# Optimization experiments

Hardware: AMD Instinct MI355X
Metric: run time of the kernel (lower is better)

The kernel has to match this reference:

```python
import jax, jax.numpy as jnp
import numpy as np

L, D, H, HD, FF, V, NH, S = 5, 1024, 8, 128, 4096, 2048, 15, 2
EPS = 1e-6
THETA = 10000.0


def rms_norm(x, w):
    x32 = x.astype(jnp.float32)
    y = x32 * jax.lax.rsqrt(jnp.mean(x32 * x32, axis=-1, keepdims=True) + EPS)
    return (y * w.astype(jnp.float32)).astype(x.dtype)


def rotate_half(x):
    x1, x2 = x[..., : HD // 2], x[..., HD // 2:]
    return jnp.concatenate((-x2, x1), axis=-1)


def setup_inputs() -> dict:
    key = jax.random.key(0)
    ks = jax.random.split(key, 20)
    s = 0.02
    inp = {
        "past_hidden": jax.random.normal(ks[0], (1, 1, D), jnp.float32),
        "cb0_token": jax.random.randint(ks[1], (1, 1), 0, V, jnp.int32),
        "codec_emb": jax.random.normal(ks[2], (V, D), jnp.float32) * s,
        "Wq": jax.random.normal(ks[3], (L, D, H * HD), jnp.float32) * s,
        "Wk": jax.random.normal(ks[4], (L, D, H * HD), jnp.float32) * s,
        "Wv": jax.random.normal(ks[5], (L, D, H * HD), jnp.float32) * s,
        "Wo": jax.random.normal(ks[6], (L, H * HD, D), jnp.float32) * s,
        "q_norm_w": jnp.ones((L, HD), jnp.float32),
        "k_norm_w": jnp.ones((L, HD), jnp.float32),
        "ln1_w": jnp.ones((L, D), jnp.float32),
        "ln2_w": jnp.ones((L, D), jnp.float32),
        "Wgate": jax.random.normal(ks[7], (L, D, FF), jnp.float32) * s,
        "Wup": jax.random.normal(ks[8], (L, D, FF), jnp.float32) * s,
        "Wdown": jax.random.normal(ks[9], (L, FF, D), jnp.float32) * s,
        "final_norm_w": jnp.ones((D,), jnp.float32),
        "lm_heads": jax.random.normal(ks[10], (NH, D, V), jnp.float32) * s,
    }
    return inp


def reference(past_hidden, codec_emb, Wq, Wk, Wv, Wo, q_norm_w, k_norm_w,
              ln1_w, ln2_w, Wgate, Wup, Wdown, final_norm_w, lm_heads,
              cb0_token):
    # Embed CB0 token and build 2-token prefill sequence [1, 2, D].
    cb0_embed = codec_emb[cb0_token]            # [1, 1, D]
    h = jnp.concatenate([past_hidden, cb0_embed], axis=1)

    # Rotary cos/sin for positions [0, 1]: [1, 1, S, HD].
    pos = jnp.arange(S, dtype=jnp.float32)
    inv_freq = 1.0 / (THETA ** (jnp.arange(0, HD, 2, dtype=jnp.float32) / HD))
    freqs = pos[:, None] * inv_freq[None, :]    # [S, HD/2]
    emb = jnp.concatenate([freqs, freqs], axis=-1)
    cos = jnp.cos(emb)[None, None]
    sin = jnp.sin(emb)[None, None]

    causal_mask = jnp.array([[0.0, -1e9], [0.0, 0.0]], jnp.float32)
    scale = 1.0 / np.sqrt(HD)

    def layer_step(h, p):
        wq, wk, wv, wo, qn, kn, l1, l2, wg, wu, wd = p
        res = h
        x = rms_norm(h, l1)                     # [1, S, D]
        q = (x @ wq).reshape(1, S, H, HD)
        k = (x @ wk).reshape(1, S, H, HD)
        v = (x @ wv).reshape(1, S, H, HD)
        q = rms_norm(q, qn)                     # per-head qk-norm
        k = rms_norm(k, kn)
        q = q.transpose(0, 2, 1, 3)             # [1, H, S, HD]
        k = k.transpose(0, 2, 1, 3)
        v = v.transpose(0, 2, 1, 3)
        q = q * cos + rotate_half(q) * sin
        k = k * cos + rotate_half(k) * sin
        attn = jnp.einsum('bhqd,bhkd->bhqk', q, k) * scale + causal_mask
        w = jax.nn.softmax(attn.astype(jnp.float32), axis=-1).astype(q.dtype)
        o = jnp.einsum('bhqk,bhkd->bhqd', w, v)
        o = o.transpose(0, 2, 1, 3).reshape(1, S, H * HD) @ wo
        h = res + o
        res = h
        x = rms_norm(h, l2)
        mlp = (jax.nn.silu(x @ wg) * (x @ wu)) @ wd
        return res + mlp, (k, v)

    h, (ks_, vs_) = jax.lax.scan(
        layer_step, h,
        (Wq, Wk, Wv, Wo, q_norm_w, k_norm_w, ln1_w, ln2_w, Wgate, Wup, Wdown))

    h = rms_norm(h, final_norm_w)
    last = h[:, -1, :]                          # [1, D]
    all_logits = jnp.einsum('bd,ndv->nbv', last, lm_heads)  # [15, 1, V]
    # Interleave keys/values per layer: [2L, 1, H, S, HD].
    kv_cache = jnp.stack([ks_, vs_], axis=1).reshape(2 * L, 1, H, S, HD)
    return all_logits, kv_cache
```

## Files before the change

kernel.cpp:

```cpp
#include <hip/hip_runtime.h>
#include <math.h>

#define EPS 1e-6f
#define FLAGS_OFF 32768


__device__ __forceinline__ float ato(const float* p) {
    return __hip_atomic_load(p, __ATOMIC_RELAXED, __HIP_MEMORY_SCOPE_AGENT);
}

__device__ __forceinline__ float red32(float v) {
#pragma unroll
    for (int m = 16; m >= 1; m >>= 1) v += __shfl_xor(v, m, 64);
    return v;
}

__device__ __forceinline__ void spin_wait(int* flags, int p, int need, int t) {
    if (t < 64) {
        int* base = flags + p * 256;
        while (true) {
            int v = (t < 16) ? __hip_atomic_load(base + t * 16, __ATOMIC_RELAXED,
                                                 __HIP_MEMORY_SCOPE_AGENT) : 0;
#pragma unroll
            for (int m = 8; m >= 1; m >>= 1) v += __shfl_xor(v, m, 64);
            v = __shfl(v, 0, 64);
            if (v >= need) break;
            __builtin_amdgcn_s_sleep(4);
        }
    }
    __syncthreads();
}

__device__ __forceinline__ void task_done(int* flags, int p, int t) {
    asm volatile("s_waitcnt vmcnt(0)" ::: "memory");
    __syncthreads();
    if (t == 0)
        __hip_atomic_fetch_add(flags + p * 256 + (blockIdx.x & 15) * 16, 1,
                               __ATOMIC_RELAXED, __HIP_MEMORY_SCOPE_AGENT);
}

__global__ void init_kernel(const float* __restrict__ past_hidden,
                            const float* __restrict__ codec_emb,
                            const int* __restrict__ tok,
                            float* __restrict__ ws,
                            float* __restrict__ logits)
{
    size_t idx = (size_t)blockIdx.x * blockDim.x + threadIdx.x;
    size_t stride = (size_t)gridDim.x * blockDim.x;
    for (size_t i = idx; i < 30720; i += stride) ws[2048 + i] = 0.f;
    for (size_t i = idx; i < 81920; i += stride) ws[43008 + i] = 0.f;
    for (size_t i = idx; i < 30720; i += stride) logits[i] = 0.f;
    int* flags = (int*)(ws + FLAGS_OFF);
    for (size_t i = idx; i < 20 * 256; i += stride) flags[i] = 0;
    int t = tok[0];
    for (size_t i = idx; i < 1024; i += stride) {
        ws[i]        = past_hidden[i];
        ws[1024 + i] = codec_emb[(size_t)t * 1024 + i];
    }
}

template <int S, int R>
__device__ void phase_gemv(
    float* smem, int t,
    const float* __restrict__ hbuf,
    const float* __restrict__ nw,
    const float* __restrict__ W0, const float* __restrict__ W1,
    const float* __restrict__ W2, size_t w_zstride,
    float* __restrict__ out, int out_sstride, size_t out_zstride, int N,
    int nx, int ny, int nz,
    int* flags, int widx, int wneed, int didx, int start, int nblk)
{
    float* xs = smem;
    float* sstot = smem + S * 1024;
    const int lane = t & 63;
    const int dp = t >> 6;
    const int ntask = nx * ny * nz;
    bool waited = (widx < 0);

    for (int task = (blockIdx.x - start + 2 * nblk) % nblk; task < ntask; task += nblk) {
        const int z = task / (nx * ny);
        const int rem = task - z * (nx * ny);
        const int by = rem / nx;
        const int bx = rem - by * nx;

        const float* W;
        if (W1) W = (z == 0) ? W0 : ((z == 1) ? W1 : W2);
        else    W = W0 + (size_t)z * w_zstride;
        float* outz = out + (size_t)z * out_zstride;

        const int j = bx * 256 + lane * 4;
        const int d0 = by * (4 * R) + dp * R;

        float4 wreg[R];
        const float* Wp = W + (size_t)d0 * N + j;
#pragma unroll
        for (int i = 0; i < R; ++i)
            wreg[i] = *reinterpret_cast<const float4*>(Wp + (size_t)i * N);

        if (!waited) { spin_wait(flags, widx, wneed, t); waited = true; }

        float ss[S];
        {
            float4 nw4 = *reinterpret_cast<const float4*>(nw + t * 4);
#pragma unroll
            for (int s = 0; s < S; ++s) {
                float x0 = ato(hbuf + s * 1024 + t * 4 + 0);
                float x1 = ato(hbuf + s * 1024 + t * 4 + 1);
                float x2 = ato(hbuf + s * 1024 + t * 4 + 2);
                float x3 = ato(hbuf + s * 1024 + t * 4 + 3);
                ss[s] = x0 * x0 + x1 * x1 + x2 * x2 + x3 * x3;
                xs[s * 1024 + t * 4 + 0] = x0 * nw4.x;
                xs[s * 1024 + t * 4 + 1] = x1 * nw4.y;
                xs[s * 1024 + t * 4 + 2] = x2 * nw4.z;
                xs[s * 1024 + t * 4 + 3] = x3 * nw4.w;
            }
        }
        __syncthreads();

        float acc[S][4];
#pragma unroll
        for (int s = 0; s < S; ++s) { acc[s][0] = acc[s][1] = acc[s][2] = acc[s][3] = 0.f; }
#pragma unroll
        for (int i = 0; i < R; ++i) {
            int dd = d0 + i;
#pragma unroll
            for (int s = 0; s < S; ++s) {
                float xv = xs[s * 1024 + dd];
                acc[s][0] += xv * wreg[i].x; acc[s][1] += xv * wreg[i].y;
                acc[s][2] += xv * wreg[i].z; acc[s][3] += xv * wreg[i].w;
            }
        }

#pragma unroll
        for (int s = 0; s < S; ++s) {
            float v = ss[s];
#pragma unroll
            for (int m = 32; m >= 1; m >>= 1) v += __shfl_xor(v, m, 64);
            if (lane == 0) sstot[s * 4 + dp] = v;
        }
        __syncthreads();
        float sc[S];
#pragma unroll
        for (int s = 0; s < S; ++s) {
            float tot = sstot[s * 4 + 0] + sstot[s * 4 + 1] + sstot[s * 4 + 2] + sstot[s * 4 + 3];
            sc[s] = rsqrtf(tot / 1024.f + EPS);
        }

#pragma unroll
        for (int s = 0; s < S; ++s)
#pragma unroll
            for (int c = 0; c < 4; ++c)
                xs[(dp * S + s) * 256 + lane * 4 + c] = acc[s][c] * sc[s];
        __syncthreads();
        for (int o = t; o < S * 256; o += 256) {
            int s = o >> 8;
            int col = o & 255;
            float sum = 0.f;
#pragma unroll
            for (int p = 0; p < 4; ++p) sum += xs[(p * S + s) * 256 + col];
            atomicAdd(outz + (size_t)s * out_sstride + bx * 256 + col, sum);
        }
        if (didx >= 0) task_done(flags, didx, t);
        else __syncthreads();
    }
}

__device__ void phase_attn_o(
    float* smem, int t,
    const float* __restrict__ qkv, const float* __restrict__ qnw,
    const float* __restrict__ knw, const float* __restrict__ W,
    float* __restrict__ out, float* __restrict__ kvc,
    int* flags, int widx, int wneed, int didx, int start, int nblk)
{
    float* xs = smem;
    const int lane = t & 63;
    const int dp = t >> 6;
    bool waited = false;

    for (int task = (blockIdx.x - start + 2 * nblk) % nblk; task < 512; task += nblk) {
        const int bx = task & 3;
        const int by = task >> 2;
        const int j = bx * 256 + lane * 4;
        const int d0 = by * 8 + dp * 2;

        float4 wreg[2];
        const float* Wp = W + (size_t)d0 * 1024 + j;
        wreg[0] = *reinterpret_cast<const float4*>(Wp);
        wreg[1] = *reinterpret_cast<const float4*>(Wp + 1024);

        if (!waited) { spin_wait(flags, widx, wneed, t); waited = true; }

        const int hh = t >> 5;
        const int g = t & 31;
        float q[2][4], k[2][4], v[2][4];
#pragma unroll
        for (int s = 0; s < 2; ++s)
#pragma unroll
            for (int c = 0; c < 4; ++c) {
                int d = g + c * 32;
                q[s][c] = ato(qkv + s * 3072 +        hh * 128 + d);
                k[s][c] = ato(qkv + s * 3072 + 1024 + hh * 128 + d);
                v[s][c] = ato(qkv + s * 3072 + 2048 + hh * 128 + d);
            }
#pragma unroll
        for (int s = 0; s < 2; ++s) {
            float sq = q[s][0]*q[s][0] + q[s][1]*q[s][1] + q[s][2]*q[s][2] + q[s][3]*q[s][3];
            float sk = k[s][0]*k[s][0] + k[s][1]*k[s][1] + k[s][2]*k[s][2] + k[s][3]*k[s][3];
            sq = red32(sq); sk = red32(sk);
            float qsc = rsqrtf(sq / 128.f + EPS);
            float ksc = rsqrtf(sk / 128.f + EPS);
#pragma unroll
            for (int c = 0; c < 4; ++c) {
                q[s][c] *= qsc * qnw[g + c * 32];
                k[s][c] *= ksc * knw[g + c * 32];
            }
        }
        float inv0 = powf(10000.f, -(float)g / 64.f);
        float inv1 = powf(10000.f, -(float)(g + 32) / 64.f);
        float cA = cosf(inv0), sA = sinf(inv0);
        float cB = cosf(inv1), sB = sinf(inv1);
        float q1[4] = { q[1][0]*cA - q[1][2]*sA, q[1][1]*cB - q[1][3]*sB,
                        q[1][2]*cA + q[1][0]*sA, q[1][3]*cB + q[1][1]*sB };
        float k1[4] = { k[1][0]*cA - k[1][2]*sA, k[1][1]*cB - k[1][3]*sB,
                        k[1][2]*cA + k[1][0]*sA, k[1][3]*cB + k[1][1]*sB };

        if (task == 0) {
#pragma unroll
            for (int c = 0; c < 4; ++c) {
                int d = g + c * 32;
                kvc[hh * 256 +       d] = k[0][c];
                kvc[hh * 256 + 128 + d] = k1[c];
                kvc[2048 + hh * 256 +       d] = v[0][c];
                kvc[2048 + hh * 256 + 128 + d] = v[1][c];
            }
        }

        float p00 = red32(q[0][0]*k[0][0] + q[0][1]*k[0][1] + q[0][2]*k[0][2] + q[0][3]*k[0][3]);
        float p01 = red32(q[0][0]*k1[0]   + q[0][1]*k1[1]   + q[0][2]*k1[2]   + q[0][3]*k1[3]);
        float p10 = red32(q1[0]*k[0][0]   + q1[1]*k[0][1]   + q1[2]*k[0][2]   + q1[3]*k[0][3]);
        float p11 = red32(q1[0]*k1[0]     + q1[1]*k1[1]     + q1[2]*k1[2]     + q1[3]*k1[3]);

        const float scale = 0.08838834764831845f;
        float s00 = p00 * scale, s01 = p01 * scale - 1e9f;
        float m0 = fmaxf(s00, s01);
        float e0 = expf(s00 - m0), e1 = expf(s01 - m0);
        float in0 = 1.f / (e0 + e1);
        float w00 = e0 * in0, w01 = e1 * in0;
        float s10 = p10 * scale, s11 = p11 * scale;
        float m1 = fmaxf(s10, s11);
        float f0 = expf(s10 - m1), f1 = expf(s11 - m1);
        float in1 = 1.f / (f0 + f1);
        float w10 = f0 * in1, w11 = f1 * in1;

#pragma unroll
        for (int c = 0; c < 4; ++c) {
            int d = g + c * 32;
            xs[       hh * 128 + d] = w00 * v[0][c] + w01 * v[1][c];
            xs[1024 + hh * 128 + d] = w10 * v[0][c] + w11 * v[1][c];
        }
        __syncthreads();

        float acc[2][4] = {{0.f,0.f,0.f,0.f},{0.f,0.f,0.f,0.f}};
#pragma unroll
        for (int i = 0; i < 2; ++i) {
            int dd = d0 + i;
#pragma unroll
            for (int s = 0; s < 2; ++s) {
                float xv = xs[s * 1024 + dd];
                acc[s][0] += xv * wreg[i].x; acc[s][1] += xv * wreg[i].y;
                acc[s][2] += xv * wreg[i].z; acc[s][3] += xv * wreg[i].w;
            }
        }
        __syncthreads();
#pragma unroll
        for (int s = 0; s < 2; ++s)
#pragma unroll
            for (int c = 0; c < 4; ++c)
                xs[(dp * 2 + s) * 256 + lane * 4 + c] = acc[s][c];
        __syncthreads();
        for (int o = t; o < 512; o += 256) {
            int s = o >> 8, col = o & 255;
            float sum = 0.f;
#pragma unroll
            for (int p = 0; p < 4; ++p) sum += xs[(p * 2 + s) * 256 + col];
            atomicAdd(out + (size_t)s * 1024 + bx * 256 + col, sum);
        }
        task_done(flags, didx, t);
    }
}

__device__ void phase_down(
    float* smem, int t,
    const float* __restrict__ gu, const float* __restrict__ W,
    float* __restrict__ out,
    int* flags, int widx, int wneed, int didx, int start, int nblk)
{
    float* red = smem;
    float* a   = smem + 2048;
    const int lane = t & 63;
    const int dp = t >> 6;
    bool waited = false;

    for (int task = (blockIdx.x - start + 2 * nblk) % nblk; task < 512; task += nblk) {
        const int bx = task & 3;
        const int by = task >> 2;
        const int j = bx * 256 + lane * 4;
        const int f0 = by * 32 + dp * 8;

        float4 wreg[8];
        const float* Wp = W + (size_t)f0 * 1024 + j;
#pragma unroll
        for (int i = 0; i < 8; ++i)
            wreg[i] = *reinterpret_cast<const float4*>(Wp + (size_t)i * 1024);

        if (!waited) { spin_wait(flags, widx, wneed, t); waited = true; }

        if (t < 64) {
            int s = t >> 5, x = t & 31;
            int f = by * 32 + x;
            float g = ato(gu + s * 8192 + f);
            float u = ato(gu + s * 8192 + 4096 + f);
            a[s * 32 + x] = g / (1.f + expf(-g)) * u;
        }
        __syncthreads();

        float acc[2][4] = {{0.f,0.f,0.f,0.f},{0.f,0.f,0.f,0.f}};
#pragma unroll
        for (int i = 0; i < 8; ++i) {
            int dl = dp * 8 + i;
#pragma unroll
            for (int s = 0; s < 2; ++s) {
                float xv = a[s * 32 + dl];
                acc[s][0] += xv * wreg[i].x; acc[s][1] += xv * wreg[i].y;
                acc[s][2] += xv * wreg[i].z; acc[s][3] += xv * wreg[i].w;
            }
        }
        __syncthreads();
#pragma unroll
        for (int s = 0; s < 2; ++s)
#pragma unroll
            for (int c = 0; c < 4; ++c)
                red[(dp * 2 + s) * 256 + lane * 4 + c] = acc[s][c];
        __syncthreads();
        for (int o = t; o < 512; o += 256) {
            int s = o >> 8, col = o & 255;
            float sum = 0.f;
#pragma unroll
            for (int p = 0; p < 4; ++p) sum += red[(p * 2 + s) * 256 + col];
            atomicAdd(out + (size_t)s * 1024 + bx * 256 + col, sum);
        }
        task_done(flags, didx, t);
    }
}

__global__ __launch_bounds__(256, 4) void net_kernel(
    const float* __restrict__ Wq, const float* __restrict__ Wk,
    const float* __restrict__ Wv, const float* __restrict__ Wo,
    const float* __restrict__ qnw, const float* __restrict__ knw,
    const float* __restrict__ ln1, const float* __restrict__ ln2,
    const float* __restrict__ Wg, const float* __restrict__ Wu,
    const float* __restrict__ Wd, const float* __restrict__ fnw,
    const float* __restrict__ lmh,
    float* __restrict__ ws, float* __restrict__ logits, float* __restrict__ kvc)
{
    __shared__ float smem[2112];
    const int t = threadIdx.x;
    const int nblk = gridDim.x;
    float* h    = ws;
    float* qkvb = ws + 2048;
    float* gub  = ws + 43008;
    int* flags  = (int*)(ws + FLAGS_OFF);
    int off = 0;

    for (int l = 0; l < 5; ++l) {
        const float* wq = Wq + (size_t)l * 1024 * 1024;
        const float* wk = Wk + (size_t)l * 1024 * 1024;
        const float* wv = Wv + (size_t)l * 1024 * 1024;
        const float* wo = Wo + (size_t)l * 1024 * 1024;
        const float* wg = Wg + (size_t)l * 1024 * 4096;
        const float* wu = Wu + (size_t)l * 1024 * 4096;
        const float* wd = Wd + (size_t)l * 4096 * 1024;
        float* qkv = qkvb + l * 6144;
        float* gu  = gub  + l * 16384;
        int st;

        st = off % nblk; off += 384;
        phase_gemv<2, 8>(smem, t, h, ln1 + l * 1024, wq, wk, wv, 0,
                         qkv, 3072, 1024, 1024, 4, 32, 3,
                         flags, l ? 4 * (l - 1) + 3 : -1, 512, 4 * l, st, nblk);
        st = off % nblk; off += 512;
        phase_attn_o(smem, t, qkv, qnw + l * 128, knw + l * 128, wo, h,
                     kvc + (size_t)(2 * l) * 2048,
                     flags, 4 * l, 384, 4 * l + 1, st, nblk);
        st = off % nblk; off += 512;
        phase_gemv<2, 16>(smem, t, h, ln2 + l * 1024, wg, wu, wu, 0,
                          gu, 8192, 4096, 4096, 16, 16, 2,
                          flags, 4 * l + 1, 512, 4 * l + 2, st, nblk);
        st = off % nblk; off += 512;
        phase_down(smem, t, gu, wd, h, flags, 4 * l + 2, 512, 4 * l + 3, st, nblk);
    }

    int st = off % nblk;
    phase_gemv<1, 16>(smem, t, h + 1024, fnw, lmh, nullptr, nullptr,
                      (size_t)1024 * 2048, logits, 2048, 2048, 2048,
                      8, 16, 15, flags, 19, 512, -1, st, nblk);
}

extern "C" void kernel_launch(void* const* d_in, const int* in_sizes, int n_in,
                              void* d_out, int out_size, void* d_ws, size_t ws_size,
                              hipStream_t stream)
{
    const float* past_hidden = (const float*)d_in[0];
    const int*   cb0         = (const int*)d_in[1];
    const float* codec_emb   = (const float*)d_in[2];
    const float* Wq  = (const float*)d_in[3];
    const float* Wk  = (const float*)d_in[4];
    const float* Wv  = (const float*)d_in[5];
    const float* Wo  = (const float*)d_in[6];
    const float* qnw = (const float*)d_in[7];
    const float* knw = (const float*)d_in[8];
    const float* ln1 = (const float*)d_in[9];
    const float* ln2 = (const float*)d_in[10];
    const float* Wg  = (const float*)d_in[11];
    const float* Wu  = (const float*)d_in[12];
    const float* Wd  = (const float*)d_in[13];
    const float* fnw = (const float*)d_in[14];
    const float* lmh = (const float*)d_in[15];

    float* ws     = (float*)d_ws;
    float* logits = (float*)d_out;
    float* kvc    = (float*)d_out + 30720;

    init_kernel<<<128, 256, 0, stream>>>(past_hidden, codec_emb, cb0, ws, logits);

    static int nblk = 0;
    if (nblk == 0) {
        int perCU = 0;
        if (hipOccupancyMaxActiveBlocksPerMultiprocessor(&perCU, net_kernel, 256, 0) != hipSuccess
            || perCU < 1) perCU = 1;
        nblk = perCU * 256;
        if (nblk > 1024) nblk = 1024;
        if (nblk < 256) nblk = 256;
    }

    void* args[] = {
        (void*)&Wq, (void*)&Wk, (void*)&Wv, (void*)&Wo,
        (void*)&qnw, (void*)&knw, (void*)&ln1, (void*)&ln2,
        (void*)&Wg, (void*)&Wu, (void*)&Wd, (void*)&fnw, (void*)&lmh,
        (void*)&ws, (void*)&logits, (void*)&kvc
    };
    hipLaunchCooperativeKernel((void*)net_kernel, dim3(nblk), dim3(256),
                               args, 0, stream);
}
```

Before: 566.1 us.

## Switch to dynamic atomic task queues with coarser tiles and split partial residual buffers

Replaces the static round-robin task assignment with per-phase atomic work counters, so blocks claim tasks dynamically. Tiles grow in the QKV, O-projection and down-projection phases, which cuts the number of tasks and flag increments. Residual updates from O and down are split into two partial buffers that later readers sum, spreading atomic contention. The cooperative launch with an occupancy query becomes a plain launch of 1024 blocks and the spin sleep is shortened. This relies on every block in the plain launch being resident to avoid spin-wait deadlock, and the residual bookkeeping through h plus hp needs care to stay correct.

```diff
diff --git a/kernel.cpp b/kernel.cpp
--- a/kernel.cpp
+++ b/kernel.cpp
@@ -2,8 +2,9 @@
 #include <math.h>
 
 #define EPS 1e-6f
-#define FLAGS_OFF 32768
-
+
+#define SYNC_OFF 32768
+#define HP_OFF   38912
 
 __device__ __forceinline__ float ato(const float* p) {
     return __hip_atomic_load(p, __ATOMIC_RELAXED, __HIP_MEMORY_SCOPE_AGENT);
@@ -15,9 +16,9 @@
     return v;
 }
 
-__device__ __forceinline__ void spin_wait(int* flags, int p, int need, int t) {
+__device__ __forceinline__ void spin_wait(int* sync, int widx, int need, int t) {
     if (t < 64) {
-        int* base = flags + p * 256;
+        int* base = sync + 1024 + widx * 256;
         while (true) {
             int v = (t < 16) ? __hip_atomic_load(base + t * 16, __ATOMIC_RELAXED,
                                                  __HIP_MEMORY_SCOPE_AGENT) : 0;
@@ -25,17 +26,17 @@
             for (int m = 8; m >= 1; m >>= 1) v += __shfl_xor(v, m, 64);
             v = __shfl(v, 0, 64);
             if (v >= need) break;
-            __builtin_amdgcn_s_sleep(4);
+            __builtin_amdgcn_s_sleep(1);
         }
     }
     __syncthreads();
 }
 
-__device__ __forceinline__ void task_done(int* flags, int p, int t) {
+__device__ __forceinline__ void task_done(int* sync, int p, int t) {
     asm volatile("s_waitcnt vmcnt(0)" ::: "memory");
     __syncthreads();
     if (t == 0)
-        __hip_atomic_fetch_add(flags + p * 256 + (blockIdx.x & 15) * 16, 1,
+        __hip_atomic_fetch_add(sync + 1024 + p * 256 + (blockIdx.x & 15) * 16, 1,
                                __ATOMIC_RELAXED, __HIP_MEMORY_SCOPE_AGENT);
 }
 
@@ -50,8 +51,9 @@
     for (size_t i = idx; i < 30720; i += stride) ws[2048 + i] = 0.f;
     for (size_t i = idx; i < 81920; i += stride) ws[43008 + i] = 0.f;
     for (size_t i = idx; i < 30720; i += stride) logits[i] = 0.f;
-    int* flags = (int*)(ws + FLAGS_OFF);
-    for (size_t i = idx; i < 20 * 256; i += stride) flags[i] = 0;
+    for (size_t i = idx; i < 4096;  i += stride) ws[HP_OFF + i] = 0.f;
+    int* sync = (int*)(ws + SYNC_OFF);
+    for (size_t i = idx; i < 6144; i += stride) sync[i] = 0;
     int t = tok[0];
     for (size_t i = idx; i < 1024; i += stride) {
         ws[i]        = past_hidden[i];
@@ -62,14 +64,15 @@
 template <int S, int R>
 __device__ void phase_gemv(
     float* smem, int t,
-    const float* __restrict__ hbuf,
+    const float* hbuf, const float* hp,
     const float* __restrict__ nw,
     const float* __restrict__ W0, const float* __restrict__ W1,
     const float* __restrict__ W2, size_t w_zstride,
     float* __restrict__ out, int out_sstride, size_t out_zstride, int N,
     int nx, int ny, int nz,
-    int* flags, int widx, int wneed, int didx, int start, int nblk)
-{
+    int* sync, int phase, int widx, int wneed, int didx)
+{
+    __shared__ int tsk;
     float* xs = smem;
     float* sstot = smem + S * 1024;
     const int lane = t & 63;
@@ -77,7 +80,14 @@
     const int ntask = nx * ny * nz;
     bool waited = (widx < 0);
 
-    for (int task = (blockIdx.x - start + 2 * nblk) % nblk; task < ntask; task += nblk) {
+    while (true) {
+        if (t == 0)
+            tsk = __hip_atomic_fetch_add(sync + phase * 16, 1, __ATOMIC_RELAXED,
+                                         __HIP_MEMORY_SCOPE_AGENT);
+        __syncthreads();
+        const int task = tsk;
+        if (task >= ntask) break;
+
         const int z = task / (nx * ny);
         const int rem = task - z * (nx * ny);
         const int by = rem / nx;
@@ -97,22 +107,29 @@
         for (int i = 0; i < R; ++i)
             wreg[i] = *reinterpret_cast<const float4*>(Wp + (size_t)i * N);
 
-        if (!waited) { spin_wait(flags, widx, wneed, t); waited = true; }
+        if (!waited) { spin_wait(sync, widx, wneed, t); waited = true; }
 
         float ss[S];
         {
             float4 nw4 = *reinterpret_cast<const float4*>(nw + t * 4);
 #pragma unroll
             for (int s = 0; s < S; ++s) {
-                float x0 = ato(hbuf + s * 1024 + t * 4 + 0);
-                float x1 = ato(hbuf + s * 1024 + t * 4 + 1);
-                float x2 = ato(hbuf + s * 1024 + t * 4 + 2);
-                float x3 = ato(hbuf + s * 1024 + t * 4 + 3);
+                int base = s * 1024 + t * 4;
+                float x0 = ato(hbuf + base + 0);
+                float x1 = ato(hbuf + base + 1);
+                float x2 = ato(hbuf + base + 2);
+                float x3 = ato(hbuf + base + 3);
+                if (hp) {
+                    x0 += ato(hp + base + 0) + ato(hp + 2048 + base + 0);
+                    x1 += ato(hp + base + 1) + ato(hp + 2048 + base + 1);
+                    x2 += ato(hp + base + 2) + ato(hp + 2048 + base + 2);
+                    x3 += ato(hp + base + 3) + ato(hp + 2048 + base + 3);
+                }
                 ss[s] = x0 * x0 + x1 * x1 + x2 * x2 + x3 * x3;
-                xs[s * 1024 + t * 4 + 0] = x0 * nw4.x;
-                xs[s * 1024 + t * 4 + 1] = x1 * nw4.y;
-                xs[s * 1024 + t * 4 + 2] = x2 * nw4.z;
-                xs[s * 1024 + t * 4 + 3] = x3 * nw4.w;
+                xs[base + 0] = x0 * nw4.x;
+                xs[base + 1] = x1 * nw4.y;
+                xs[base + 2] = x2 * nw4.z;
+                xs[base + 3] = x3 * nw4.w;
             }
         }
         __syncthreads();
@@ -160,7 +177,7 @@
             for (int p = 0; p < 4; ++p) sum += xs[(p * S + s) * 256 + col];
             atomicAdd(outz + (size_t)s * out_sstride + bx * 256 + col, sum);
         }
-        if (didx >= 0) task_done(flags, didx, t);
+        if (didx >= 0) task_done(sync, didx, t);
         else __syncthreads();
     }
 }
@@ -169,26 +186,37 @@
     float* smem, int t,
     const float* __restrict__ qkv, const float* __restrict__ qnw,
     const float* __restrict__ knw, const float* __restrict__ W,
-    float* __restrict__ out, float* __restrict__ kvc,
-    int* flags, int widx, int wneed, int didx, int start, int nblk)
-{
+    float* __restrict__ hp,
+    float* __restrict__ kvc,
+    int* sync, int phase, int widx, int wneed, int didx)
+{
+    __shared__ int tsk;
     float* xs = smem;
     const int lane = t & 63;
     const int dp = t >> 6;
     bool waited = false;
 
-    for (int task = (blockIdx.x - start + 2 * nblk) % nblk; task < 512; task += nblk) {
+    while (true) {
+        if (t == 0)
+            tsk = __hip_atomic_fetch_add(sync + phase * 16, 1, __ATOMIC_RELAXED,
+                                         __HIP_MEMORY_SCOPE_AGENT);
+        __syncthreads();
+        const int task = tsk;
+        if (task >= 128) break;
+
         const int bx = task & 3;
         const int by = task >> 2;
         const int j = bx * 256 + lane * 4;
-        const int d0 = by * 8 + dp * 2;
-
-        float4 wreg[2];
+        const int d0 = by * 32 + dp * 8;
+        float* out = hp + (by & 1) * 2048;
+
+        float4 wreg[8];
         const float* Wp = W + (size_t)d0 * 1024 + j;
-        wreg[0] = *reinterpret_cast<const float4*>(Wp);
-        wreg[1] = *reinterpret_cast<const float4*>(Wp + 1024);
-
-        if (!waited) { spin_wait(flags, widx, wneed, t); waited = true; }
+#pragma unroll
+        for (int i = 0; i < 8; ++i)
+            wreg[i] = *reinterpret_cast<const float4*>(Wp + (size_t)i * 1024);
+
+        if (!waited) { spin_wait(sync, widx, wneed, t); waited = true; }
 
         const int hh = t >> 5;
         const int g = t & 31;
@@ -262,7 +290,7 @@
 
         float acc[2][4] = {{0.f,0.f,0.f,0.f},{0.f,0.f,0.f,0.f}};
 #pragma unroll
-        for (int i = 0; i < 2; ++i) {
+        for (int i = 0; i < 8; ++i) {
             int dd = d0 + i;
 #pragma unroll
             for (int s = 0; s < 2; ++s) {
@@ -285,52 +313,61 @@
             for (int p = 0; p < 4; ++p) sum += xs[(p * 2 + s) * 256 + col];
             atomicAdd(out + (size_t)s * 1024 + bx * 256 + col, sum);
         }
-        task_done(flags, didx, t);
+        task_done(sync, didx, t);
     }
 }
 
 __device__ void phase_down(
     float* smem, int t,
     const float* __restrict__ gu, const float* __restrict__ W,
-    float* __restrict__ out,
-    int* flags, int widx, int wneed, int didx, int start, int nblk)
-{
+    float* __restrict__ hp,
+    int* sync, int phase, int widx, int wneed, int didx)
+{
+    __shared__ int tsk;
     float* red = smem;
     float* a   = smem + 2048;
     const int lane = t & 63;
     const int dp = t >> 6;
     bool waited = false;
 
-    for (int task = (blockIdx.x - start + 2 * nblk) % nblk; task < 512; task += nblk) {
+    while (true) {
+        if (t == 0)
+            tsk = __hip_atomic_fetch_add(sync + phase * 16, 1, __ATOMIC_RELAXED,
+                                         __HIP_MEMORY_SCOPE_AGENT);
+        __syncthreads();
+        const int task = tsk;
+        if (task >= 256) break;
+
         const int bx = task & 3;
         const int by = task >> 2;
         const int j = bx * 256 + lane * 4;
-        const int f0 = by * 32 + dp * 8;
-
-        float4 wreg[8];
+        const int f0 = by * 64 + dp * 16;
+        float* out = hp + (by & 1) * 2048;
+
+        float4 wreg[16];
         const float* Wp = W + (size_t)f0 * 1024 + j;
 #pragma unroll
-        for (int i = 0; i < 8; ++i)
+        for (int i = 0; i < 16; ++i)
             wreg[i] = *reinterpret_cast<const float4*>(Wp + (size_t)i * 1024);
 
-        if (!waited) { spin_wait(flags, widx, wneed, t); waited = true; }
-
-        if (t < 64) {
-            int s = t >> 5, x = t & 31;
-            int f = by * 32 + x;
+        if (!waited) { spin_wait(sync, widx, wneed, t); waited = true; }
+
+        if (t < 128) {
+            int s = t >> 6, x = t & 63;
+            int f = by * 64 + x;
             float g = ato(gu + s * 8192 + f);
             float u = ato(gu + s * 8192 + 4096 + f);
-            a[s * 32 + x] = g / (1.f + expf(-g)) * u;
+            a[s * 64 + x] = g / (1.f + expf(-g)) * u;
         }
         __syncthreads();
 
         float acc[2][4] = {{0.f,0.f,0.f,0.f},{0.f,0.f,0.f,0.f}};
 #pragma unroll
-        for (int i = 0; i < 8; ++i) {
-            int dl = dp * 8 + i;
+        for (int i = 0; i < 16; ++i) {
+            int dl = dp * 16 + i;
 #pragma unroll
             for (int s = 0; s < 2; ++s) {
-                float xv = a[s * 32 + dl];
+                float xv = a[s * 64 + dl];
                 acc[s][0] += xv * wreg[i].x; acc[s][1] += xv * wreg[i].y;
                 acc[s][2] += xv * wreg[i].z; acc[s][3] += xv * wreg[i].w;
             }
@@ -349,7 +386,7 @@
             for (int p = 0; p < 4; ++p) sum += red[(p * 2 + s) * 256 + col];
             atomicAdd(out + (size_t)s * 1024 + bx * 256 + col, sum);
         }
-        task_done(flags, didx, t);
+        task_done(sync, didx, t);
     }
 }
 
@@ -363,14 +400,13 @@
     const float* __restrict__ lmh,
     float* __restrict__ ws, float* __restrict__ logits, float* __restrict__ kvc)
 {
-    __shared__ float smem[2112];
+    __shared__ float smem[2176];
     const int t = threadIdx.x;
-    const int nblk = gridDim.x;
     float* h    = ws;
     float* qkvb = ws + 2048;
+    float* hp   = ws + HP_OFF;
     float* gub  = ws + 43008;
-    int* flags  = (int*)(ws + FLAGS_OFF);
-    int off = 0;
+    int* sync   = (int*)(ws + SYNC_OFF);
 
     for (int l = 0; l < 5; ++l) {
         const float* wq = Wq + (size_t)l * 1024 * 1024;
@@ -382,28 +418,23 @@
         const float* wd = Wd + (size_t)l * 4096 * 1024;
         float* qkv = qkvb + l * 6144;
         float* gu  = gub  + l * 16384;
-        int st;
-
-        st = off % nblk; off += 384;
-        phase_gemv<2, 8>(smem, t, h, ln1 + l * 1024, wq, wk, wv, 0,
-                         qkv, 3072, 1024, 1024, 4, 32, 3,
-                         flags, l ? 4 * (l - 1) + 3 : -1, 512, 4 * l, st, nblk);
-        st = off % nblk; off += 512;
-        phase_attn_o(smem, t, qkv, qnw + l * 128, knw + l * 128, wo, h,
+
+        phase_gemv<2, 16>(smem, t, h, hp, ln1 + l * 1024, wq, wk, wv, 0,
+                          qkv, 3072, 1024, 1024, 4, 16, 3,
+                          sync, 4 * l, l ? 4 * (l - 1) + 3 : -1, 256, 4 * l);
+        phase_attn_o(smem, t, qkv, qnw + l * 128, knw + l * 128, wo, hp,
                      kvc + (size_t)(2 * l) * 2048,
-                     flags, 4 * l, 384, 4 * l + 1, st, nblk);
-        st = off % nblk; off += 512;
-        phase_gemv<2, 16>(smem, t, h, ln2 + l * 1024, wg, wu, wu, 0,
+                     sync, 4 * l + 1, 4 * l, 192, 4 * l + 1);
+        phase_gemv<2, 16>(smem, t, h, hp, ln2 + l * 1024, wg, wu, wu, 0,
                           gu, 8192, 4096, 4096, 16, 16, 2,
-                          flags, 4 * l + 1, 512, 4 * l + 2, st, nblk);
-        st = off % nblk; off += 512;
-        phase_down(smem, t, gu, wd, h, flags, 4 * l + 2, 512, 4 * l + 3, st, nblk);
-    }
-
-    int st = off % nblk;
-    phase_gemv<1, 16>(smem, t, h + 1024, fnw, lmh, nullptr, nullptr,
+                          sync, 4 * l + 2, 4 * l + 1, 128, 4 * l + 2);
+        phase_down(smem, t, gu, wd, hp,
+                   sync, 4 * l + 3, 4 * l + 2, 512, 4 * l + 3);
+    }
+
+    phase_gemv<1, 16>(smem, t, h + 1024, hp + 1024, fnw, lmh, nullptr, nullptr,
                       (size_t)1024 * 2048, logits, 2048, 2048, 2048,
-                      8, 16, 15, flags, 19, 512, -1, st, nblk);
+                      8, 16, 15, sync, 20, 19, 256, -1);
 }
 
 extern "C" void kernel_launch(void* const* d_in, const int* in_sizes, int n_in,
@@ -433,22 +464,7 @@
 
     init_kernel<<<128, 256, 0, stream>>>(past_hidden, codec_emb, cb0, ws, logits);
 
-    static int nblk = 0;
-    if (nblk == 0) {
-        int perCU = 0;
-        if (hipOccupancyMaxActiveBlocksPerMultiprocessor(&perCU, net_kernel, 256, 0) != hipSuccess
-            || perCU < 1) perCU = 1;
-        nblk = perCU * 256;
-        if (nblk > 1024) nblk = 1024;
-        if (nblk < 256) nblk = 256;
-    }
-
-    void* args[] = {
-        (void*)&Wq, (void*)&Wk, (void*)&Wv, (void*)&Wo,
-        (void*)&qnw, (void*)&knw, (void*)&ln1, (void*)&ln2,
-        (void*)&Wg, (void*)&Wu, (void*)&Wd, (void*)&fnw, (void*)&lmh,
-        (void*)&ws, (void*)&logits, (void*)&kvc
-    };
-    hipLaunchCooperativeKernel((void*)net_kernel, dim3(nblk), dim3(256),
-                               args, 0, stream);
-}
+    net_kernel<<<1024, 256, 0, stream>>>(
+        Wq, Wk, Wv, Wo, qnw, knw, ln1, ln2, Wg, Wu, Wd, fnw, lmh,
+        ws, logits, kvc);
+}
```

Measured after the change: 874.0 us. +54.4%, slower.
